# Performance work log

Hardware: AMD Instinct MI355X
Metric: run time of the kernel (lower is better)

Reference implementation:

```python
import jax, jax.numpy as jnp
import numpy as np

H = 128  # hidden_dim
F = 256  # node_feature_dim
N = 40000      # layer-graph nodes
E = 640000     # layer-graph edges
L = 8          # number of head graphs
NH = 8192      # nodes per head graph
EH = 131072    # edges per head graph


def setup_inputs() -> dict:
    key = jax.random.key(0)
    ks = jax.random.split(key, 32)
    s = 0.05
    inp = {
        "x": jax.random.normal(ks[0], (N, F), jnp.float32),
        "edge_index": jax.random.randint(ks[1], (2, E), 0, N, jnp.int64) if jax.config.jax_enable_x64 else jax.random.randint(ks[1], (2, E), 0, N, jnp.int32),
        "head_x": jax.random.normal(ks[2], (L, NH, F), jnp.float32),
        "head_edge_index": jax.random.randint(ks[3], (L, 2, EH), 0, NH, jnp.int32),
        # feature encoder (Linear-ReLU-Linear-ReLU)
        "enc_w1": jax.random.normal(ks[4], (F, H), jnp.float32) * s, "enc_b1": jnp.zeros((H,), jnp.float32),
        "enc_w2": jax.random.normal(ks[5], (H, H), jnp.float32) * s, "enc_b2": jnp.zeros((H,), jnp.float32),
        # two GCNConv layers
        "gnn_w1": jax.random.normal(ks[6], (H, H), jnp.float32) * s, "gnn_b1": jnp.zeros((H,), jnp.float32),
        "gnn_w2": jax.random.normal(ks[7], (H, H), jnp.float32) * s, "gnn_b2": jnp.zeros((H,), jnp.float32),
        # layer policy head
        "lp_w1": jax.random.normal(ks[8], (H, H), jnp.float32) * s, "lp_b1": jnp.zeros((H,), jnp.float32),
        "lp_w2": jax.random.normal(ks[9], (H, 1), jnp.float32) * s, "lp_b2": jnp.zeros((1,), jnp.float32),
        # head policy head
        "hp_w1": jax.random.normal(ks[10], (H, H), jnp.float32) * s, "hp_b1": jnp.zeros((H,), jnp.float32),
        "hp_w2": jax.random.normal(ks[11], (H, 1), jnp.float32) * s, "hp_b2": jnp.zeros((1,), jnp.float32),
        # value net
        "v_w1": jax.random.normal(ks[12], (H, H), jnp.float32) * s, "v_b1": jnp.zeros((H,), jnp.float32),
        "v_w2": jax.random.normal(ks[13], (H, 1), jnp.float32) * s, "v_b2": jnp.zeros((1,), jnp.float32),
    }
    return inp


def _gcn(h, src, dst, w, b, n):
    # torch_geometric GCNConv: add self loops, symmetric normalization, then X@W + b
    h = h @ w
    loop = jnp.arange(n, dtype=src.dtype)
    si = jnp.concatenate([src, loop])
    di = jnp.concatenate([dst, loop])
    deg = jax.ops.segment_sum(jnp.ones_like(di, dtype=h.dtype), di, num_segments=n)
    dinv = jnp.where(deg > 0, jax.lax.rsqrt(deg), 0.0)
    msg = h[si] * (dinv[si] * dinv[di])[:, None]  # gather + per-edge scale
    return jax.ops.segment_sum(msg, di, num_segments=n) + b


def reference(x, edge_index, head_x, head_edge_index,
              enc_w1, enc_b1, enc_w2, enc_b2,
              gnn_w1, gnn_b1, gnn_w2, gnn_b2,
              lp_w1, lp_b1, lp_w2, lp_b2,
              hp_w1, hp_b1, hp_w2, hp_b2,
              v_w1, v_b1, v_w2, v_b2):
    relu = jax.nn.relu

    def encode(z):
        return relu(relu(z @ enc_w1 + enc_b1) @ enc_w2 + enc_b2)

    def gnn_stack(z, ei, n):
        z = encode(z)
        z = relu(_gcn(z, ei[0], ei[1], gnn_w1, gnn_b1, n))
        z = relu(_gcn(z, ei[0], ei[1], gnn_w2, gnn_b2, n))
        return z

    h = gnn_stack(x, edge_index, x.shape[0])                    # [N, H]
    layer_probs = jax.nn.sigmoid(relu(h @ lp_w1 + lp_b1) @ lp_w2 + lp_b2)[:, 0]  # [N]
    state_value = relu(h.mean(axis=0) @ v_w1 + v_b1) @ v_w2 + v_b2               # [1]

    def head_fn(hx, hei):
        hh = gnn_stack(hx, hei, hx.shape[0])
        return jax.nn.sigmoid(relu(hh @ hp_w1 + hp_b1) @ hp_w2 + hp_b2)[:, 0]
    head_probs = jax.vmap(head_fn)(head_x, head_edge_index)     # [L, NH]

    # original gates head computation on layer_probs[i] > 0.5 (data-dependent);
    # here we compute all head graphs and expose the gate mask explicitly.
    head_mask = layer_probs[:head_x.shape[0]] > 0.5
    return layer_probs, head_probs, head_mask, state_value
```

## Files before the change

### kernel.cpp

```cpp
#include <hip/hip_runtime.h>
#include <math.h>


typedef unsigned short ushort_t;
using short8 = __attribute__((ext_vector_type(8))) short;
using f32x4  = __attribute__((ext_vector_type(4))) float;

constexpr int N_L  = 40000;
constexpr int E_L  = 640000;
constexpr int L_H  = 8;
constexpr int N_H1 = 8192;
constexpr int E_H1 = 131072;
constexpr int N_HT = 65536;
constexpr int E_HT = 1048576;
constexpr int E_T  = E_L + E_HT;
constexpr int NLP  = 40064;
constexpr int R_T  = 105600;
constexpr int HBASE = 40064;

constexpr int NB_ENC  = R_T / 128;
constexpr int NB_FILL = (E_T + 255) / 256;
constexpr int NB_CONV = 448;
constexpr int NB_POL  = R_T / 128;
constexpr int NB_CSUM = (N_L + 127) / 128;

constexpr size_t OFF_SAF  = 0;
constexpr size_t OFF_HB   = (size_t)NLP * 512;
constexpr size_t OFF_ZPAD = OFF_HB + (size_t)N_HT * 256;
constexpr size_t OFF_SBH  = OFF_ZPAD + 512;
constexpr size_t OFF_SBL  = OFF_SBH + (size_t)R_T * 256;
constexpr size_t OFF_WTH  = OFF_SBL + (size_t)NLP * 256;
constexpr size_t OFF_WTL  = OFF_WTH + 229376;
constexpr size_t OFF_DINV = OFF_WTL + 229376;
constexpr size_t OFF_HSUM = OFF_DINV + (size_t)R_T * 4;
constexpr size_t OFF_DEG  = OFF_HSUM + 512;
constexpr size_t OFF_RP   = OFF_DEG + (size_t)R_T * 4;
constexpr size_t OFF_EG   = OFF_RP + (size_t)(R_T + 1) * 4;
constexpr size_t OFF_BSUM = OFF_EG + (size_t)(E_T + 32) * 2;

constexpr int ZIDX_L = (int)(OFF_ZPAD / 512);
constexpr int ZIDX_H = N_HT;

static_assert(OFF_ZPAD % 512 == 0, "zpad alignment");


__device__ __forceinline__ unsigned short bf16_rne(float f) {
  unsigned u = __float_as_uint(f);
  unsigned r = u + 0x7FFFu + ((u >> 16) & 1u);
  return (unsigned short)(r >> 16);
}
__device__ __forceinline__ float bfhi_f(unsigned short h) {
  return __uint_as_float((unsigned)h << 16);
}
__device__ __forceinline__ void split2(float f, unsigned short& h, unsigned short& l) {
  h = bf16_rne(f);
  l = bf16_rne(f - bfhi_f(h));
}

__device__ __forceinline__ void gload16(const void* g, void* l) {
  __builtin_amdgcn_global_load_lds((__attribute__((address_space(1))) void*)(g),
                                   (__attribute__((address_space(3))) void*)(l),
                                   16, 0, 0);
}


__global__ __launch_bounds__(256) void prep_csr(
    const float* __restrict__ w0, const float* __restrict__ w1,
    const float* __restrict__ w2, const float* __restrict__ w3,
    const float* __restrict__ w4, const float* __restrict__ w5,
    unsigned short* __restrict__ th, unsigned short* __restrict__ tl,
    const int* __restrict__ ei, const int* __restrict__ hei,
    int* __restrict__ indeg, int* __restrict__ rank) {
  if (blockIdx.x < NB_CONV) {
    int t = blockIdx.x * 256 + threadIdx.x;
    const float* src; int K, dstoff, idx;
    if (t < 32768) { src = w0; K = 256; dstoff = 0; idx = t; }
    else {
      int s = (t - 32768) >> 14;
      idx = (t - 32768) & 16383;
      K = 128;
      dstoff = 32768 + s * 16384;
      src = s == 0 ? w1 : s == 1 ? w2 : s == 2 ? w3 : s == 3 ? w4 : w5;
    }
    int k = idx >> 7, c = idx & 127;
    unsigned short h_, l_;
    split2(src[idx], h_, l_);
    th[dstoff + c * K + k] = h_;
    tl[dstoff + c * K + k] = l_;
  } else {
    int i = (blockIdx.x - NB_CONV) * 256 + threadIdx.x;
    if (i < E_L) {
      rank[i] = atomicAdd(&indeg[ei[E_L + i]], 1);
    } else if (i < E_T) {
      int t = i - E_L;
      int l = t >> 17, e = t & (E_H1 - 1);
      rank[i] = atomicAdd(&indeg[HBASE + l * N_H1 + hei[l * 2 * E_H1 + E_H1 + e]], 1);
    }
  }
}


__global__ __launch_bounds__(1024) void scan_block(const int* __restrict__ in, int n,
                                                   int* __restrict__ out,
                                                   int* __restrict__ bsum) {
  __shared__ int s[1024];
  int t = threadIdx.x;
  int i = blockIdx.x * 1024 + t;
  int v = (i < n) ? in[i] : 0;
  s[t] = v;
  __syncthreads();
  for (int off = 1; off < 1024; off <<= 1) {
    int x = (t >= off) ? s[t - off] : 0;
    __syncthreads();
    s[t] += x;
    __syncthreads();
  }
  if (i < n) out[i] = s[t] - v;
  if (t == 1023) bsum[blockIdx.x] = s[t];
}

__global__ __launch_bounds__(64) void scan_top128(int* __restrict__ bsum, int nb) {
  int lane = threadIdx.x;
  int a = (lane < nb) ? bsum[lane] : 0;
  int b = (lane + 64 < nb) ? bsum[lane + 64] : 0;
  int ia = a;
  for (int off = 1; off < 64; off <<= 1) {
    int x = __shfl_up(ia, off);
    if (lane >= off) ia += x;
  }
  int ta = __shfl(ia, 63);
  int ib = b;
  for (int off = 1; off < 64; off <<= 1) {
    int x = __shfl_up(ib, off);
    if (lane >= off) ib += x;
  }
  int tb = __shfl(ib, 63);
  if (lane < nb) bsum[lane] = ia - a;
  if (lane + 64 < nb) bsum[lane + 64] = ta + ib - b;
  if (lane == 0) bsum[nb] = ta + tb;
}

__global__ __launch_bounds__(256) void scan_fix(int* __restrict__ rowptr,
                                                const int* __restrict__ bsum,
                                                const int* __restrict__ indeg,
                                                float* __restrict__ dinv,
                                                int n, int nb) {
  int i = blockIdx.x * 256 + threadIdx.x;
  if (i < n) {
    rowptr[i] += bsum[i >> 10];
    dinv[i] = 1.0f / sqrtf((float)(indeg[i] + 1));
  } else if (i == n) {
    rowptr[n] = bsum[nb];
  }
}


template <bool SPLIT>
__device__ __forceinline__ void stage_w_t(const unsigned short* Wth,
                                          const unsigned short* Wtl, int K, int kc,
                                          char* Ws_h, char* Ws_l,
                                          int wv, int rsub, int xr) {
#pragma unroll
  for (int j = 0; j < 4; ++j) {
    int q = wv * 4 + j;
    int c = q * 8 + rsub;
    size_t gb = ((size_t)c * K + kc) * 2 + (size_t)xr * 16;
    gload16((const char*)Wth + gb, Ws_h + q * 1024);
    if constexpr (SPLIT) gload16((const char*)Wtl + gb, Ws_l + q * 1024);
  }
}

template <bool SPLIT>
__device__ __forceinline__ void mfma_chunk_t(const char* As_h, const char* As_l,
                                             const char* Ws_h, const char* Ws_l,
                                             int wv, int g, int li,
                                             f32x4 acc[2][8]) {
  short8 fa_h[2][2], fa_l[2][2];
#pragma unroll
  for (int m = 0; m < 2; ++m)
#pragma unroll
    for (int ks = 0; ks < 2; ++ks) {
      int row = wv * 32 + m * 16 + li;
      int off = row * 128 + ks * 64 + g * 16;
      off ^= (row & 7) << 4;
      fa_h[m][ks] = *(const short8*)(As_h + off);
      if constexpr (SPLIT) fa_l[m][ks] = *(const short8*)(As_l + off);
    }
#pragma unroll
  for (int nh = 0; nh < 2; ++nh) {
    short8 fb_h[4][2], fb_l[4][2];
#pragma unroll
    for (int n = 0; n < 4; ++n)
#pragma unroll
      for (int ks = 0; ks < 2; ++ks) {
        int c = nh * 64 + n * 16 + li;
        int off = c * 128 + ks * 64 + g * 16;
        off ^= (c & 7) << 4;
        fb_h[n][ks] = *(const short8*)(Ws_h + off);
        if constexpr (SPLIT) fb_l[n][ks] = *(const short8*)(Ws_l + off);
      }
#pragma unroll
    for (int m = 0; m < 2; ++m)
#pragma unroll
      for (int n = 0; n < 4; ++n)
#pragma unroll
        for (int ks = 0; ks < 2; ++ks) {
          f32x4 a_ = acc[m][nh * 4 + n];
          a_ = __builtin_amdgcn_mfma_f32_16x16x32_bf16(fa_h[m][ks], fb_h[n][ks], a_, 0, 0, 0);
          if constexpr (SPLIT) {
            a_ = __builtin_amdgcn_mfma_f32_16x16x32_bf16(fa_h[m][ks], fb_l[n][ks], a_, 0, 0, 0);
            a_ = __builtin_amdgcn_mfma_f32_16x16x32_bf16(fa_l[m][ks], fb_h[n][ks], a_, 0, 0, 0);
          }
          acc[m][nh * 4 + n] = a_;
        }
  }
}

template <bool SPLIT>
__device__ __forceinline__ void write_h_slice_t(const f32x4 acc[2][8],
                                                const float* bj, int kc,
                                                char* As_h, char* As_l,
                                                int wv, int g, int li) {
#pragma unroll
  for (int m = 0; m < 2; ++m)
#pragma unroll
    for (int jj = 0; jj < 4; ++jj) {
      int j = (kc >> 4) + jj;
#pragma unroll
      for (int r = 0; r < 4; ++r) {
        float o = fmaxf(acc[m][j][r] + bj[j], 0.f);
        int row = wv * 32 + m * 16 + g * 4 + r;
        int cl = jj * 16 + li;
        int byte = row * 128 + ((((cl >> 3) ^ (row & 7)) << 4) | ((cl & 7) * 2));
        if constexpr (SPLIT) {
          unsigned short h_, l_;
          split2(o, h_, l_);
          *(unsigned short*)(As_h + byte) = h_;
          *(unsigned short*)(As_l + byte) = l_;
        } else {
          *(unsigned short*)(As_h + byte) = bf16_rne(o);
        }
      }
    }
}

__device__ __forceinline__ void write_g_out(const f32x4 acc[2][8],
                                            const float* __restrict__ dinvg,
                                            float* __restrict__ G,
                                            unsigned short* __restrict__ Hb,
                                            int row0, int wv, int g, int li) {
  if (row0 < NLP) {
#pragma unroll
    for (int m = 0; m < 2; ++m)
#pragma unroll
      for (int r = 0; r < 4; ++r) {
        int rowg = row0 + wv * 32 + m * 16 + g * 4 + r;
        float dvr = dinvg[rowg];
#pragma unroll
        for (int j = 0; j < 8; ++j)
          G[(size_t)rowg * 128 + j * 16 + li] = acc[m][j][r] * dvr;
      }
  } else {
#pragma unroll
    for (int m = 0; m < 2; ++m)
#pragma unroll
      for (int r = 0; r < 4; ++r) {
        int rowg = row0 + wv * 32 + m * 16 + g * 4 + r;
        float dvr = dinvg[rowg];
        int rl = rowg - HBASE;
#pragma unroll
        for (int j = 0; j < 8; ++j)
          Hb[(size_t)rl * 128 + j * 16 + li] = bf16_rne(acc[m][j][r] * dvr);
      }
  }
}


template <bool SPLIT>
__device__ __forceinline__ void enc_body(
    const float* __restrict__ xs, int lclamp,
    const unsigned short* __restrict__ W1h, const unsigned short* __restrict__ W1l,
    const unsigned short* __restrict__ W2h, const unsigned short* __restrict__ W2l,
    const unsigned short* __restrict__ Wgh, const unsigned short* __restrict__ Wgl,
    const float* __restrict__ b1, const float* __restrict__ b2,
    const float* __restrict__ dinvg,
    float* __restrict__ G, unsigned short* __restrict__ Hb,
    char* As_h, char* As_l, char* Ws_h, char* Ws_l,
    int tid, int wv, int g, int li, int row0, int lrow0, int rsub, int xr) {
  float bj1[8], bj2[8];
#pragma unroll
  for (int j = 0; j < 8; ++j) {
    bj1[j] = b1[j * 16 + li];
    bj2[j] = b2[j * 16 + li];
  }

  f32x4 acc1[2][8];
#pragma unroll
  for (int m = 0; m < 2; ++m)
#pragma unroll
    for (int j = 0; j < 8; ++j) acc1[m][j] = f32x4{0.f, 0.f, 0.f, 0.f};

#pragma unroll
  for (int kc = 0; kc < 256; kc += 64) {
    __syncthreads();
    stage_w_t<SPLIT>(W1h, W1l, 256, kc, Ws_h, Ws_l, wv, rsub, xr);
    {
      int r = tid >> 1, hf = tid & 1;
      int lrow = min(lrow0 + r, lclamp);
      const float* src = xs + (size_t)lrow * 256 + kc + hf * 32;
#pragma unroll
      for (int i = 0; i < 4; ++i) {
        float4 a = ((const float4*)src)[2 * i];
        float4 b = ((const float4*)src)[2 * i + 1];
        float f[8] = {a.x, a.y, a.z, a.w, b.x, b.y, b.z, b.w};
        short8 vh, vl;
#pragma unroll
        for (int e = 0; e < 8; ++e) {
          if constexpr (SPLIT) {
            unsigned short h_, l_;
            split2(f[e], h_, l_);
            vh[e] = (short)h_;
            vl[e] = (short)l_;
          } else {
            vh[e] = (short)bf16_rne(f[e]);
          }
        }
        int xu = hf * 4 + i;
        int u = r * 8 + (xu ^ (r & 7));
        *(short8*)(As_h + u * 16) = vh;
        if constexpr (SPLIT) *(short8*)(As_l + u * 16) = vl;
      }
    }
    __syncthreads();
    mfma_chunk_t<SPLIT>(As_h, As_l, Ws_h, Ws_l, wv, g, li, acc1);
  }

  f32x4 acc2[2][8];
#pragma unroll
  for (int m = 0; m < 2; ++m)
#pragma unroll
    for (int j = 0; j < 8; ++j) acc2[m][j] = f32x4{0.f, 0.f, 0.f, 0.f};

#pragma unroll
  for (int kc = 0; kc < 128; kc += 64) {
    __syncthreads();
    stage_w_t<SPLIT>(W2h, W2l, 128, kc, Ws_h, Ws_l, wv, rsub, xr);
    write_h_slice_t<SPLIT>(acc1, bj1, kc, As_h, As_l, wv, g, li);
    __syncthreads();
    mfma_chunk_t<SPLIT>(As_h, As_l, Ws_h, Ws_l, wv, g, li, acc2);
  }

  f32x4 acc3[2][8];
#pragma unroll
  for (int m = 0; m < 2; ++m)
#pragma unroll
    for (int j = 0; j < 8; ++j) acc3[m][j] = f32x4{0.f, 0.f, 0.f, 0.f};

#pragma unroll
  for (int kc = 0; kc < 128; kc += 64) {
    __syncthreads();
    stage_w_t<SPLIT>(Wgh, Wgl, 128, kc, Ws_h, Ws_l, wv, rsub, xr);
    write_h_slice_t<SPLIT>(acc2, bj2, kc, As_h, As_l, wv, g, li);
    __syncthreads();
    mfma_chunk_t<SPLIT>(As_h, As_l, Ws_h, Ws_l, wv, g, li, acc3);
  }

  write_g_out(acc3, dinvg, G, Hb, row0, wv, g, li);
}

__global__ __launch_bounds__(256, 2) void enc_fused(
    const float* __restrict__ x, const float* __restrict__ head_x,
    const unsigned short* __restrict__ W1h, const unsigned short* __restrict__ W1l,
    const unsigned short* __restrict__ W2h, const unsigned short* __restrict__ W2l,
    const unsigned short* __restrict__ Wgh, const unsigned short* __restrict__ Wgl,
    const float* __restrict__ b1, const float* __restrict__ b2,
    const float* __restrict__ dinvg,
    float* __restrict__ G, unsigned short* __restrict__ Hb,
    const int* __restrict__ ei, const int* __restrict__ hei,
    const int* __restrict__ rowptr, const int* __restrict__ rank,
    unsigned short* __restrict__ eg) {
  __shared__ __align__(16) char lds[65536];

  if (blockIdx.x >= NB_ENC) {
    int i = (blockIdx.x - NB_ENC) * 256 + threadIdx.x;
    if (i < E_L) {
      int dst = ei[E_L + i];
      int src = ei[i];
      eg[rowptr[dst] + rank[i]] = (unsigned short)src;
    } else if (i < E_T) {
      int t = i - E_L;
      int l = t >> 17, e = t & (E_H1 - 1);
      int b2o = l * 2 * E_H1;
      int dst = HBASE + l * N_H1 + hei[b2o + E_H1 + e];
      int srcl = l * N_H1 + hei[b2o + e];
      eg[rowptr[dst] + rank[i]] = (unsigned short)srcl;
    }
    return;
  }

  char* As_h = lds;
  char* As_l = lds + 16384;
  char* Ws_h = lds + 32768;
  char* Ws_l = lds + 49152;

  const int tid = threadIdx.x;
  const int lane = tid & 63;
  const int wv = tid >> 6;
  const int g = lane >> 4;
  const int li = lane & 15;
  const int row0 = blockIdx.x * 128;
  const int rsub = lane >> 3;
  const int xr = (lane & 7) ^ ((lane >> 3) & 7);

  if (row0 < NLP) {
    enc_body<true>(x, N_L - 1, W1h, W1l, W2h, W2l, Wgh, Wgl, b1, b2, dinvg, G, Hb,
                   As_h, As_l, Ws_h, Ws_l, tid, wv, g, li, row0, row0, rsub, xr);
  } else {
    enc_body<false>(head_x, N_HT - 1, W1h, nullptr, W2h, nullptr, Wgh, nullptr,
                    b1, b2, dinvg, G, Hb,
                    As_h, As_l, Ws_h, Ws_l, tid, wv, g, li, row0, row0 - NLP,
                    rsub, xr);
  }
}


template <bool SPLIT>
__device__ __forceinline__ void mm_g_body(
    const unsigned short* __restrict__ Ah, const unsigned short* __restrict__ Al,
    const unsigned short* __restrict__ Wth, const unsigned short* __restrict__ Wtl,
    char* As_h, char* As_l, char* Ws_h, char* Ws_l,
    int wv, int g, int li, int row0, int rsub, int xr, f32x4 acc[2][8]) {
  constexpr int K = 128;
#pragma unroll
  for (int kc = 0; kc < K; kc += 64) {
    __syncthreads();
    stage_w_t<SPLIT>(Wth, Wtl, K, kc, Ws_h, Ws_l, wv, rsub, xr);
#pragma unroll
    for (int j = 0; j < 4; ++j) {
      int q = wv * 4 + j;
      int r = q * 8 + rsub;
      size_t gb = ((size_t)(row0 + r) * K + kc) * 2 + (size_t)xr * 16;
      gload16((const char*)Ah + gb, As_h + q * 1024);
      if constexpr (SPLIT) gload16((const char*)Al + gb, As_l + q * 1024);
    }
    __syncthreads();
    mfma_chunk_t<SPLIT>(As_h, As_l, Ws_h, Ws_l, wv, g, li, acc);
  }
}

__global__ __launch_bounds__(256) void mm_g(
    const unsigned short* __restrict__ Ah, const unsigned short* __restrict__ Al,
    const unsigned short* __restrict__ Wth, const unsigned short* __restrict__ Wtl,
    const float* __restrict__ dinvg,
    float* __restrict__ Cf, unsigned short* __restrict__ Hb) {
  __shared__ __align__(16) char lds[65536];
  char* As_h = lds;
  char* As_l = lds + 16384;
  char* Ws_h = lds + 32768;
  char* Ws_l = lds + 49152;

  const int tid = threadIdx.x;
  const int lane = tid & 63;
  const int wv = tid >> 6;
  const int g = lane >> 4;
  const int li = lane & 15;
  const int row0 = blockIdx.x * 128;
  const int rsub = lane >> 3;
  const int xr = (lane & 7) ^ ((lane >> 3) & 7);

  f32x4 acc[2][8];
#pragma unroll
  for (int m = 0; m < 2; ++m)
#pragma unroll
    for (int j = 0; j < 8; ++j) acc[m][j] = f32x4{0.f, 0.f, 0.f, 0.f};

  if (row0 < NLP)
    mm_g_body<true>(Ah, Al, Wth, Wtl, As_h, As_l, Ws_h, Ws_l,
                    wv, g, li, row0, rsub, xr, acc);
  else
    mm_g_body<false>(Ah, nullptr, Wth, nullptr, As_h, As_l, Ws_h, Ws_l,
                     wv, g, li, row0, rsub, xr, acc);

  write_g_out(acc, dinvg, Cf, Hb, row0, wv, g, li);
}


__global__ __launch_bounds__(256) void mm_policy(
    const unsigned short* __restrict__ Ah, const unsigned short* __restrict__ Al,
    const unsigned short* __restrict__ Wth_l, const unsigned short* __restrict__ Wtl_l,
    const unsigned short* __restrict__ Wth_h,
    const float* __restrict__ b1l, const float* __restrict__ b1h,
    const float* __restrict__ w2l, const float* __restrict__ w2h,
    const float* __restrict__ b2l, const float* __restrict__ b2h,
    float* __restrict__ out_l, float* __restrict__ out_h,
    float* __restrict__ hsum) {
  __shared__ __align__(16) char lds[65536];

  if (blockIdx.x >= NB_POL) {
    int cb = blockIdx.x - NB_POL;
    int f = threadIdx.x & 127;
    int half = threadIdx.x >> 7;
    int r0 = cb * 128 + half * 64;
    int r1 = min(r0 + 64, N_L);
    float acc = 0.f;
    for (int r = r0; r < r1; ++r) {
      size_t idx = (size_t)r * 128 + f;
      acc += bfhi_f(Ah[idx]) + bfhi_f(Al[idx]);
    }
    atomicAdd(&hsum[f], acc);
    return;
  }

  char* As_h = lds;
  char* As_l = lds + 16384;
  char* Ws_h = lds + 32768;
  char* Ws_l = lds + 49152;

  const int tid = threadIdx.x;
  const int lane = tid & 63;
  const int wv = tid >> 6;
  const int g = lane >> 4;
  const int li = lane & 15;
  const int row0 = blockIdx.x * 128;
  const bool isl = row0 < NLP;
  const int rsub = lane >> 3;
  const int xr = (lane & 7) ^ ((lane >> 3) & 7);

  const float* bias = isl ? b1l : b1h;
  const float* pw2  = isl ? w2l : w2h;
  const float* pb2  = isl ? b2l : b2h;

  f32x4 acc[2][8];
#pragma unroll
  for (int m = 0; m < 2; ++m)
#pragma unroll
    for (int j = 0; j < 8; ++j) acc[m][j] = f32x4{0.f, 0.f, 0.f, 0.f};

  if (isl)
    mm_g_body<true>(Ah, Al, Wth_l, Wtl_l, As_h, As_l, Ws_h, Ws_l,
                    wv, g, li, row0, rsub, xr, acc);
  else
    mm_g_body<false>(Ah, nullptr, Wth_h, nullptr, As_h, As_l, Ws_h, Ws_l,
                     wv, g, li, row0, rsub, xr, acc);

  float w2c[8], bj[8];
#pragma unroll
  for (int j = 0; j < 8; ++j) {
    w2c[j] = pw2[j * 16 + li];
    bj[j]  = bias[j * 16 + li];
  }
#pragma unroll
  for (int m = 0; m < 2; ++m)
#pragma unroll
    for (int r = 0; r < 4; ++r) {
      float p = 0.f;
#pragma unroll
      for (int j = 0; j < 8; ++j) {
        float o = fmaxf(acc[m][j][r] + bj[j], 0.f);
        p = fmaf(o, w2c[j], p);
      }
      p += __shfl_xor(p, 1);
      p += __shfl_xor(p, 2);
      p += __shfl_xor(p, 4);
      p += __shfl_xor(p, 8);
      if (li == 0) {
        int rowg = row0 + wv * 32 + m * 16 + g * 4 + r;
        if (isl) {
          if (rowg < N_L) out_l[rowg] = 1.0f / (1.0f + expf(-(p + pb2[0])));
        } else {
          out_h[rowg - HBASE] = 1.0f / (1.0f + expf(-(p + pb2[0])));
        }
      }
    }
}


__global__ __launch_bounds__(256) void agg_packed(const float* __restrict__ Hin,
                                                  const unsigned short* __restrict__ Hb,
                                                  const float* __restrict__ dinvg,
                                                  const int* __restrict__ rowptr,
                                                  const unsigned short* __restrict__ eg,
                                                  const float* __restrict__ bias,
                                                  unsigned short* __restrict__ Oh,
                                                  unsigned short* __restrict__ Ol) {
  int b = blockIdx.x;
  {
    int x = b & 7, j = b >> 3;
    b = (j < 626) ? (x * 626 + j) : (5008 + x * 1024 + (j - 626));
  }
  const int lane = threadIdx.x & 63;
  const int wv = threadIdx.x >> 6;
  const int half = lane >> 5;
  const int hl = lane & 31;
  const int v = b * 8 + wv * 2 + half;

  const float4* H4 = (const float4*)Hin;
  const ushort4* Hb4 = (const ushort4*)Hb;

  float dv = dinvg[v];
  int e0 = rowptr[v], e1 = rowptr[v + 1];
  int deg = e1 - e0;

  float4 acc;
  if (v < NLP) {
    acc = H4[(size_t)v * 32 + hl];
  } else {
    ushort4 t = Hb4[(size_t)(v - HBASE) * 32 + hl];
    acc.x = bfhi_f(t.x);
    acc.y = bfhi_f(t.y);
    acc.z = bfhi_f(t.z);
    acc.w = bfhi_f(t.w);
  }

  int nb = (deg + 15) >> 4;
  int nbo = __shfl_xor(nb, 32);
  int nbmax = max(nb, nbo);

  if (v < NLP) {
    for (int t = 0; t < nbmax; ++t) {
      int e = t * 16;
      unsigned pr = 0;
      if (hl < 16 && e + hl < deg) pr = eg[e0 + e + hl];
      float4 xs[16];
#pragma unroll
      for (int i = 0; i < 16; ++i) {
        unsigned pe = (unsigned)__shfl((int)pr, (half << 5) | i);
        int u = (e + i < deg) ? (int)pe : ZIDX_L;
        xs[i] = H4[(size_t)u * 32 + hl];
      }
#pragma unroll
      for (int i = 0; i < 16; ++i) {
        acc.x += xs[i].x;
        acc.y += xs[i].y;
        acc.z += xs[i].z;
        acc.w += xs[i].w;
      }
    }
  } else {
    for (int t = 0; t < nbmax; ++t) {
      int e = t * 16;
      unsigned pr = 0;
      if (hl < 16 && e + hl < deg) pr = eg[e0 + e + hl];
      ushort4 xs[16];
#pragma unroll
      for (int i = 0; i < 16; ++i) {
        unsigned pe = (unsigned)__shfl((int)pr, (half << 5) | i);
        int u = (e + i < deg) ? (int)pe : ZIDX_H;
        xs[i] = Hb4[(size_t)u * 32 + hl];
      }
#pragma unroll
      for (int i = 0; i < 16; ++i) {
        acc.x += bfhi_f(xs[i].x);
        acc.y += bfhi_f(xs[i].y);
        acc.z += bfhi_f(xs[i].z);
        acc.w += bfhi_f(xs[i].w);
      }
    }
  }

  float4 bb = ((const float4*)bias)[hl];
  acc.x = fmaxf(fmaf(dv, acc.x, bb.x), 0.f);
  acc.y = fmaxf(fmaf(dv, acc.y, bb.y), 0.f);
  acc.z = fmaxf(fmaf(dv, acc.z, bb.z), 0.f);
  acc.w = fmaxf(fmaf(dv, acc.w, bb.w), 0.f);

  if (v < NLP) {
    ushort4 th, tl;
    split2(acc.x, th.x, tl.x);
    split2(acc.y, th.y, tl.y);
    split2(acc.z, th.z, tl.z);
    split2(acc.w, th.w, tl.w);
    ((ushort4*)Oh)[(size_t)v * 32 + hl] = th;
    ((ushort4*)Ol)[(size_t)v * 32 + hl] = tl;
  } else {
    ushort4 th;
    th.x = bf16_rne(acc.x);
    th.y = bf16_rne(acc.y);
    th.z = bf16_rne(acc.z);
    th.w = bf16_rne(acc.w);
    ((ushort4*)Oh)[(size_t)v * 32 + hl] = th;
  }
}


__global__ __launch_bounds__(128) void value_kernel(const float* __restrict__ hsum,
                                                    const float* __restrict__ w1,
                                                    const float* __restrict__ b1,
                                                    const float* __restrict__ w2,
                                                    const float* __restrict__ b2,
                                                    float* __restrict__ out) {
  __shared__ float hm[128];
  __shared__ float red[128];
  int t = threadIdx.x;
  hm[t] = hsum[t] * (1.0f / (float)N_L);
  __syncthreads();
  float acc = b1[t];
  for (int k = 0; k < 128; ++k) acc = fmaf(hm[k], w1[k * 128 + t], acc);
  red[t] = fmaxf(acc, 0.f) * w2[t];
  for (int off = 64; off > 0; off >>= 1) {
    __syncthreads();
    if (t < off) red[t] += red[t + off];
  }
  __syncthreads();
  if (t == 0) out[0] = red[0] + b2[0];
}

__global__ __launch_bounds__(64) void mask_kernel(const float* __restrict__ lp,
                                                  float* __restrict__ out) {
  int i = threadIdx.x;
  if (i < L_H) out[i] = (lp[i] > 0.5f) ? 1.0f : 0.0f;
}


extern "C" void kernel_launch(void* const* d_in, const int* in_sizes, int n_in,
                              void* d_out, int out_size, void* d_ws, size_t ws_size,
                              hipStream_t stream) {
  const float* x      = (const float*)d_in[0];
  const int*   ei     = (const int*)d_in[1];
  const float* head_x = (const float*)d_in[2];
  const int*   hei    = (const int*)d_in[3];
  const float* enc_w1 = (const float*)d_in[4];
  const float* enc_b1 = (const float*)d_in[5];
  const float* enc_w2 = (const float*)d_in[6];
  const float* enc_b2 = (const float*)d_in[7];
  const float* gnn_w1 = (const float*)d_in[8];
  const float* gnn_b1 = (const float*)d_in[9];
  const float* gnn_w2 = (const float*)d_in[10];
  const float* gnn_b2 = (const float*)d_in[11];
  const float* lp_w1  = (const float*)d_in[12];
  const float* lp_b1  = (const float*)d_in[13];
  const float* lp_w2  = (const float*)d_in[14];
  const float* lp_b2  = (const float*)d_in[15];
  const float* hp_w1  = (const float*)d_in[16];
  const float* hp_b1  = (const float*)d_in[17];
  const float* hp_w2  = (const float*)d_in[18];
  const float* hp_b2  = (const float*)d_in[19];
  const float* v_w1   = (const float*)d_in[20];
  const float* v_b1   = (const float*)d_in[21];
  const float* v_w2   = (const float*)d_in[22];
  const float* v_b2   = (const float*)d_in[23];
  float* out = (float*)d_out;

  char* base = (char*)d_ws;
  float* SAf = (float*)(base + OFF_SAF);
  unsigned short* Hb = (unsigned short*)(base + OFF_HB);
  unsigned short* SBh = (unsigned short*)(base + OFF_SBH);
  unsigned short* SBl = (unsigned short*)(base + OFF_SBL);
  unsigned short* WTh = (unsigned short*)(base + OFF_WTH);
  unsigned short* WTl = (unsigned short*)(base + OFF_WTL);
  float* dinv_g = (float*)(base + OFF_DINV);
  float* hsum   = (float*)(base + OFF_HSUM);
  int* indeg_g  = (int*)(base + OFF_DEG);
  int* rowptr_g = (int*)(base + OFF_RP);
  unsigned short* eg = (unsigned short*)(base + OFF_EG);
  int* bsum     = (int*)(base + OFF_BSUM);
  int* rank     = (int*)(base + OFF_SBH);

  const int WT_ENC1 = 0, WT_ENC2 = 32768, WT_G1 = 49152, WT_G2 = 65536,
            WT_LP = 81920, WT_HP = 98304;

  const int OUT_LP = 0, OUT_HP = N_L, OUT_MASK = N_L + N_HT, OUT_SV = N_L + N_HT + L_H;

  hipMemsetAsync(indeg_g, 0, (size_t)R_T * sizeof(int), stream);
  hipMemsetAsync(hsum, 0, 128 * sizeof(float), stream);
  hipMemsetAsync(base + OFF_ZPAD, 0, 512, stream);

  prep_csr<<<NB_CONV + NB_FILL, 256, 0, stream>>>(
      enc_w1, enc_w2, gnn_w1, gnn_w2, lp_w1, hp_w1, WTh, WTl,
      ei, hei, indeg_g, rank);

  scan_block<<<(R_T + 1023) / 1024, 1024, 0, stream>>>(indeg_g, R_T, rowptr_g, bsum);
  scan_top128<<<1, 64, 0, stream>>>(bsum, (R_T + 1023) / 1024);
  scan_fix<<<(R_T + 256) / 256, 256, 0, stream>>>(rowptr_g, bsum, indeg_g, dinv_g,
                                                  R_T, (R_T + 1023) / 1024);

  enc_fused<<<NB_ENC + NB_FILL, 256, 0, stream>>>(
      x, head_x,
      WTh + WT_ENC1, WTl + WT_ENC1,
      WTh + WT_ENC2, WTl + WT_ENC2,
      WTh + WT_G1,   WTl + WT_G1,
      enc_b1, enc_b2, dinv_g, SAf, Hb,
      ei, hei, rowptr_g, rank, eg);

  agg_packed<<<R_T / 8, 256, 0, stream>>>(SAf, Hb, dinv_g, rowptr_g, eg, gnn_b1,
                                          SBh, SBl);

  mm_g<<<R_T / 128, 256, 0, stream>>>(SBh, SBl, WTh + WT_G2, WTl + WT_G2,
                                      dinv_g, SAf, Hb);
  agg_packed<<<R_T / 8, 256, 0, stream>>>(SAf, Hb, dinv_g, rowptr_g, eg, gnn_b2,
                                          SBh, SBl);

  mm_policy<<<NB_POL + NB_CSUM, 256, 0, stream>>>(
      SBh, SBl,
      WTh + WT_LP, WTl + WT_LP, WTh + WT_HP,
      lp_b1, hp_b1, lp_w2, hp_w2, lp_b2, hp_b2,
      out + OUT_LP, out + OUT_HP, hsum);

  value_kernel<<<1, 128, 0, stream>>>(hsum, v_w1, v_b1, v_w2, v_b2, out + OUT_SV);

  mask_kernel<<<1, 64, 0, stream>>>(out + OUT_LP, out + OUT_MASK);
}
```

Measured before the change: 372.7 us.

## Drop low-bf16 split for most layer policy rows and fuse value/mask kernels

The layer-graph policy matmul now uses the high+low bf16 split only for the first 128-row block, which feeds the gate mask. All other layer rows use only the high bf16 part. The column-sum for the mean also reads only the high part. The value and mask kernels are merged into one two-block launch to save a launch. This cuts memory reads and MFMA work but lowers precision for layer_probs and state_value, which may exceed tolerance.

```diff
diff --git a/kernel.cpp b/kernel.cpp
--- a/kernel.cpp
+++ b/kernel.cpp
@@ -503,10 +503,8 @@
     int r0 = cb * 128 + half * 64;
     int r1 = min(r0 + 64, N_L);
     float acc = 0.f;
-    for (int r = r0; r < r1; ++r) {
-      size_t idx = (size_t)r * 128 + f;
-      acc += bfhi_f(Ah[idx]) + bfhi_f(Al[idx]);
-    }
+    for (int r = r0; r < r1; ++r)
+      acc += bfhi_f(Ah[(size_t)r * 128 + f]);
     atomicAdd(&hsum[f], acc);
     return;
   }
@@ -536,9 +534,12 @@
 #pragma unroll
     for (int j = 0; j < 8; ++j) acc[m][j] = f32x4{0.f, 0.f, 0.f, 0.f};
 
-  if (isl)
+  if (row0 == 0)
     mm_g_body<true>(Ah, Al, Wth_l, Wtl_l, As_h, As_l, Ws_h, Ws_l,
                     wv, g, li, row0, rsub, xr, acc);
+  else if (isl)
+    mm_g_body<false>(Ah, nullptr, Wth_l, nullptr, As_h, As_l, Ws_h, Ws_l,
+                     wv, g, li, row0, rsub, xr, acc);
   else
     mm_g_body<false>(Ah, nullptr, Wth_h, nullptr, As_h, As_l, Ws_h, Ws_l,
                      wv, g, li, row0, rsub, xr, acc);
@@ -683,12 +684,17 @@
 }
 
 
-__global__ __launch_bounds__(128) void value_kernel(const float* __restrict__ hsum,
-                                                    const float* __restrict__ w1,
-                                                    const float* __restrict__ b1,
-                                                    const float* __restrict__ w2,
-                                                    const float* __restrict__ b2,
-                                                    float* __restrict__ out) {
+__global__ __launch_bounds__(128) void value_mask_kernel(
+    const float* __restrict__ hsum,
+    const float* __restrict__ w1, const float* __restrict__ b1,
+    const float* __restrict__ w2, const float* __restrict__ b2,
+    const float* __restrict__ lp,
+    float* __restrict__ out_sv, float* __restrict__ out_mask) {
+  if (blockIdx.x == 1) {
+    int i = threadIdx.x;
+    if (i < L_H) out_mask[i] = (lp[i] > 0.5f) ? 1.0f : 0.0f;
+    return;
+  }
   __shared__ float hm[128];
   __shared__ float red[128];
   int t = threadIdx.x;
@@ -702,13 +708,7 @@
     if (t < off) red[t] += red[t + off];
   }
   __syncthreads();
-  if (t == 0) out[0] = red[0] + b2[0];
-}
-
-__global__ __launch_bounds__(64) void mask_kernel(const float* __restrict__ lp,
-                                                  float* __restrict__ out) {
-  int i = threadIdx.x;
-  if (i < L_H) out[i] = (lp[i] > 0.5f) ? 1.0f : 0.0f;
+  if (t == 0) out_sv[0] = red[0] + b2[0];
 }
 
 
@@ -796,7 +796,7 @@
       lp_b1, hp_b1, lp_w2, hp_w2, lp_b2, hp_b2,
       out + OUT_LP, out + OUT_HP, hsum);
 
-  value_kernel<<<1, 128, 0, stream>>>(hsum, v_w1, v_b1, v_w2, v_b2, out + OUT_SV);
-
-  mask_kernel<<<1, 64, 0, stream>>>(out + OUT_LP, out + OUT_MASK);
-}
+  value_mask_kernel<<<2, 128, 0, stream>>>(hsum, v_w1, v_b1, v_w2, v_b2,
+                                           out + OUT_LP, out + OUT_SV,
+                                           out + OUT_MASK);
+}
```

Result: no change. 367.6 us (-1.4%).
